# Kernel tuning notes

Measured on AMD Instinct MI355X. Metric: run time of the kernel, lower is better.

Reference implementation:

```python
import jax, jax.numpy as jnp
import numpy as np

NUM_HEADS = 8
EPS = 1e-3

N_TOKENS = 32768
DIM = 256
N_WIN = 128
WIN = N_TOKENS // N_WIN  # 256 tokens per window


def setup_inputs() -> dict:
    key = jax.random.key(0)
    ks = jax.random.split(key, 4)
    x = jax.random.normal(ks[0], (N_TOKENS, DIM), dtype=jnp.float32)
    # torch nn.Linear weights are [out_features, in_features]
    w_qkv = jax.random.normal(ks[1], (3 * DIM, DIM), dtype=jnp.float32) * (DIM ** -0.5)
    w_proj = jax.random.normal(ks[2], (DIM, DIM), dtype=jnp.float32) * (DIM ** -0.5)
    b_proj = jnp.zeros((DIM,), dtype=jnp.float32)
    batch_win_inds = (jnp.arange(N_TOKENS) // WIN).astype(jnp.int64)
    offsets = (jnp.arange(N_WIN) * WIN).astype(jnp.int64)
    counts = jnp.full((N_WIN,), WIN, dtype=jnp.int64)
    return {"x": x, "w_qkv": w_qkv, "w_proj": w_proj, "b_proj": b_proj,
            "offsets": offsets, "counts": counts, "batch_win_inds": batch_win_inds}


def reference(x, w_qkv, w_proj, b_proj, offsets, counts, batch_win_inds):
    N, C = x.shape
    H = NUM_HEADS
    hd = C // H
    W = counts.shape[0]  # number of windows (static)

    qkv = x @ w_qkv.T                      # [N, 3C]
    q, k, v = jnp.split(qkv, 3, axis=-1)   # each [N, C]
    q = jax.nn.relu(q.reshape(N, H, hd))   # [N, H, hd]
    k = jax.nn.relu(k.reshape(N, H, hd))
    v = v.reshape(N, H, hd)

    seg = batch_win_inds.astype(jnp.int32)
    # per-window KV state: kv[w] = sum_{i in w} k_i^T v_i   -> [W, H, hd, hd]
    kv = jax.ops.segment_sum(jnp.einsum('nhc,nhd->nhcd', k, v), seg, num_segments=W)
    # per-window key sum for normalizer                      -> [W, H, hd]
    s = jax.ops.segment_sum(k, seg, num_segments=W)

    y = jnp.einsum('nhc,nhcd->nhd', q, kv[seg])              # [N, H, hd]
    z = jnp.sum(s[seg] * q, axis=-1, keepdims=True)          # [N, H, 1]
    y = y / (z + EPS)

    y = y.reshape(N, C) @ w_proj.T + b_proj                  # [N, C]
    return y
```

## Files before the change

kernel.cpp:

```cpp
#include <hip/hip_runtime.h>

typedef __bf16 bf16_t;
typedef bf16_t bf16x8 __attribute__((ext_vector_type(8)));
typedef bf16_t bf16x4 __attribute__((ext_vector_type(4)));
typedef float f32x4 __attribute__((ext_vector_type(4)));

#define M_TOK 32768
#define NWIN 128
#define WIN  256

typedef __attribute__((address_space(3))) void* as3p;
typedef const __attribute__((address_space(1))) void* as1p;

__device__ __forceinline__ void gll16(const void* g, void* l) {
    __builtin_amdgcn_global_load_lds((as1p)g, (as3p)l, 16, 0, 0);
}

#define VMW_(n) asm volatile("s_waitcnt vmcnt(" #n ")" ::: "memory")
#define VMW(n) VMW_(n)

__global__ __launch_bounds__(256) void wconv(
    const float* __restrict__ wq, const float* __restrict__ wp,
    bf16_t* __restrict__ wqb, bf16_t* __restrict__ wpb)
{
    int i4 = (blockIdx.x * 256 + threadIdx.x) * 4;
    const float* s; bf16_t* dst; int idx;
    if (i4 < 196608) { s = wq; dst = wqb; idx = i4; }
    else             { s = wp; dst = wpb; idx = i4 - 196608; }
    f32x4 v = *(const f32x4*)(s + idx);
    bf16x4 o;
    o[0] = (bf16_t)v[0]; o[1] = (bf16_t)v[1]; o[2] = (bf16_t)v[2]; o[3] = (bf16_t)v[3];
    *(bf16x4*)(dst + idx) = o;
}

__global__ __launch_bounds__(512) void gemm1_qkv(
    const float* __restrict__ X,
    const bf16_t* __restrict__ Wb,
    bf16_t* __restrict__ QKV)
{
    __shared__ __align__(16) bf16_t Al[64][256];
    __shared__ __align__(16) bf16_t Bs[3][128][64];

    const int tid = threadIdx.x;
    const int lane = tid & 63;
    const int wv = tid >> 6;
    const int wm = wv >> 2, wn = wv & 3;
    const int m0 = blockIdx.x * 64;
    const int r = lane & 15, q = lane >> 4;
    const int rl = lane >> 3, gsl = lane & 7;

    f32x4 acc[2][2] = {};

    auto stageB = [&](int t) {
        const int nb = t >> 2, kc = (t & 3) * 64;
#pragma unroll
        for (int u = 0; u < 2; ++u)
            gll16(Wb + (size_t)(nb * 128 + wv * 16 + u * 8 + rl) * 256 + kc + (gsl ^ rl) * 8,
                  &Bs[t % 3][wv * 16 + u * 8][0]);
    };

    auto comp = [&](int t) {
        const int buf = t % 3;
#pragma unroll
        for (int s = 0; s < 2; ++s) {
            const int kk = (t & 3) * 2 + s;
            bf16x8 a[2], b[2];
#pragma unroll
            for (int i = 0; i < 2; ++i)
                a[i] = *(const bf16x8*)((const bf16_t*)Al +
                        (wm * 32 + i * 16 + r) * 256 + ((kk * 4 + q) ^ (r & 7)) * 8);
#pragma unroll
            for (int j = 0; j < 2; ++j)
                b[j] = *(const bf16x8*)&Bs[buf][wn * 32 + j * 16 + r][((s * 4 + q) ^ (r & 7)) * 8];
#pragma unroll
            for (int i = 0; i < 2; ++i)
#pragma unroll
                for (int j = 0; j < 2; ++j)
                    acc[i][j] = __builtin_amdgcn_mfma_f32_16x16x32_bf16(b[j], a[i], acc[i][j], 0, 0, 0);
        }
    };

    auto wout = [&](int nb) {
#pragma unroll
        for (int i = 0; i < 2; ++i) {
            const int rowg = m0 + wm * 32 + i * 16 + r;
#pragma unroll
            for (int j = 0; j < 2; ++j) {
                const int nbcol = nb * 128 + wn * 32 + j * 16 + q * 4;
                const int nblk = nbcol >> 5, d = nbcol & 31;
                bf16x4 o;
#pragma unroll
                for (int reg = 0; reg < 4; ++reg) {
                    float v = acc[i][j][reg];
                    if (nblk < 16) v = fmaxf(v, 0.0f);
                    o[reg] = (bf16_t)v;
                }
                *(bf16x4*)&QKV[((size_t)nblk * M_TOK + rowg) * 32 + d] = o;
                acc[i][j] = (f32x4){0.f, 0.f, 0.f, 0.f};
            }
        }
    };

    f32x4 av[8];
#pragma unroll
    for (int it = 0; it < 8; ++it) {
        const int L = it * 512 + tid;
        const int row = L >> 6, col4 = L & 63;
        av[it] = *(const f32x4*)(X + (size_t)(m0 + row) * 256 + col4 * 4);
    }
    __builtin_amdgcn_sched_barrier(0);
    stageB(0); stageB(1); stageB(2);
    __builtin_amdgcn_sched_barrier(0);
#pragma unroll
    for (int it = 0; it < 8; ++it) {
        const int L = it * 512 + tid;
        const int row = L >> 6, col4 = L & 63;
        bf16x4 o;
        o[0] = (bf16_t)av[it][0]; o[1] = (bf16_t)av[it][1];
        o[2] = (bf16_t)av[it][2]; o[3] = (bf16_t)av[it][3];
        const int gs = (col4 >> 1) ^ (row & 7);
        *(bf16x4*)((bf16_t*)Al + row * 256 + gs * 8 + (col4 & 1) * 4) = o;
    }
    asm volatile("s_waitcnt lgkmcnt(0)" ::: "memory");
    __builtin_amdgcn_s_barrier();

#define G1S(t, NW) do { \
        VMW(NW); \
        __builtin_amdgcn_s_barrier(); \
        __builtin_amdgcn_sched_barrier(0); \
        comp(t); \
        if (((t) & 3) == 3) wout((t) >> 2); \
        __builtin_amdgcn_sched_barrier(0); \
        __builtin_amdgcn_s_barrier(); \
        if ((t) + 3 < 24) stageB((t) + 3); \
    } while (0)

    G1S(0, 4);  G1S(1, 4);  G1S(2, 4);  G1S(3, 4);
    G1S(4, 4);  G1S(5, 4);  G1S(6, 4);  G1S(7, 4);
    G1S(8, 4);  G1S(9, 4);  G1S(10, 4); G1S(11, 4);
    G1S(12, 4); G1S(13, 4); G1S(14, 4); G1S(15, 4);
    G1S(16, 4); G1S(17, 4); G1S(18, 4); G1S(19, 4);
    G1S(20, 4); G1S(21, 4); G1S(22, 2); G1S(23, 0);
#undef G1S
}

__global__ __launch_bounds__(512) void gemm2_proj(
    const bf16_t* __restrict__ Y,
    const bf16_t* __restrict__ Wb,
    const float* __restrict__ bias,
    float* __restrict__ Out)
{
    __shared__ __align__(16) bf16_t Al[64][256];
    __shared__ __align__(16) bf16_t Bs[3][128][64];

    const int tid = threadIdx.x;
    const int lane = tid & 63;
    const int wv = tid >> 6;
    const int wm = wv >> 2, wn = wv & 3;
    const int m0 = blockIdx.x * 64;
    const int r = lane & 15, q = lane >> 4;
    const int rl = lane >> 3, gsl = lane & 7;

    f32x4 acc[2][2] = {};

    auto stageB = [&](int t) {
        const int nb = t >> 2, kc = (t & 3) * 64;
#pragma unroll
        for (int u = 0; u < 2; ++u)
            gll16(Wb + (size_t)(nb * 128 + wv * 16 + u * 8 + rl) * 256 + kc + (gsl ^ rl) * 8,
                  &Bs[t % 3][wv * 16 + u * 8][0]);
    };

    auto comp = [&](int t) {
        const int buf = t % 3;
#pragma unroll
        for (int s = 0; s < 2; ++s) {
            const int kk = (t & 3) * 2 + s;
            bf16x8 a[2], b[2];
#pragma unroll
            for (int i = 0; i < 2; ++i)
                a[i] = *(const bf16x8*)((const bf16_t*)Al +
                        (wm * 32 + i * 16 + r) * 256 + ((kk * 4 + q) ^ (r & 7)) * 8);
#pragma unroll
            for (int j = 0; j < 2; ++j)
                b[j] = *(const bf16x8*)&Bs[buf][wn * 32 + j * 16 + r][((s * 4 + q) ^ (r & 7)) * 8];
#pragma unroll
            for (int i = 0; i < 2; ++i)
#pragma unroll
                for (int j = 0; j < 2; ++j)
                    acc[i][j] = __builtin_amdgcn_mfma_f32_16x16x32_bf16(b[j], a[i], acc[i][j], 0, 0, 0);
        }
    };

    auto wout = [&](int nb) {
#pragma unroll
        for (int i = 0; i < 2; ++i) {
            const int rowg = m0 + wm * 32 + i * 16 + r;
#pragma unroll
            for (int j = 0; j < 2; ++j) {
                const int n = nb * 128 + wn * 32 + j * 16 + q * 4;
                f32x4 bi = *(const f32x4*)(bias + n);
                f32x4 o;
#pragma unroll
                for (int reg = 0; reg < 4; ++reg) o[reg] = acc[i][j][reg] + bi[reg];
                *(f32x4*)&Out[(size_t)rowg * 256 + n] = o;
                acc[i][j] = (f32x4){0.f, 0.f, 0.f, 0.f};
            }
        }
    };

#pragma unroll
    for (int u = 0; u < 4; ++u) {
        const int rowl = wv * 8 + u * 2 + (lane >> 5);
        const int gsrc = (lane & 31) ^ (rowl & 7);
        gll16(Y + (size_t)(m0 + rowl) * 256 + gsrc * 8, &Al[wv * 8 + u * 2][0]);
    }
    stageB(0); stageB(1); stageB(2);

#define G2S(t, NW) do { \
        VMW(NW); \
        __builtin_amdgcn_s_barrier(); \
        __builtin_amdgcn_sched_barrier(0); \
        comp(t); \
        if (((t) & 3) == 3) wout((t) >> 2); \
        __builtin_amdgcn_sched_barrier(0); \
        __builtin_amdgcn_s_barrier(); \
        if ((t) + 3 < 8) stageB((t) + 3); \
    } while (0)

    G2S(0, 4); G2S(1, 4); G2S(2, 4); G2S(3, 4);
    G2S(4, 4); G2S(5, 4); G2S(6, 2); G2S(7, 0);
#undef G2S
}

__global__ __launch_bounds__(256) void kvy_kernel(
    const bf16_t* __restrict__ QKV,
    const int* __restrict__ offsets,
    const int* __restrict__ counts,
    bf16_t* __restrict__ Y)
{
    const int w = blockIdx.x;
    const int h = blockIdx.y;
    const int is64 = (counts[1] == 0) ? 1 : 0;
    const int off = offsets[w << is64];
    const int tid = threadIdx.x;
    const int lane = tid & 63;
    const int wv = tid >> 6;

    __shared__ __align__(16) bf16_t KT[32 * 264];
    __shared__ __align__(16) bf16_t VT[32 * 264];
    __shared__ __align__(16) bf16_t KVT[32 * 40];
    __shared__ float sbuf[32];
    __shared__ float spart[32 * 8];
    __shared__ float zinv[WIN];

    {
        const int t = tid;
        const bf16_t* kp = QKV + ((size_t)(8 + h) * M_TOK + off + t) * 32;
        const bf16_t* vp = QKV + ((size_t)(16 + h) * M_TOK + off + t) * 32;
        bf16_t ka[32], va[32];
#pragma unroll
        for (int u = 0; u < 4; ++u) {
            bf16x8 kk = *(const bf16x8*)(kp + u * 8);
            bf16x8 vvv = *(const bf16x8*)(vp + u * 8);
#pragma unroll
            for (int j = 0; j < 8; ++j) { ka[u * 8 + j] = kk[j]; va[u * 8 + j] = vvv[j]; }
        }
#pragma unroll
        for (int c = 0; c < 32; ++c) {
            KT[c * 264 + t] = ka[c];
            VT[c * 264 + t] = va[c];
        }
    }
    __syncthreads();

    {
        const int c = tid >> 3;
        const int tc = (tid & 7) * 32;
        float ps = 0.f;
#pragma unroll
        for (int u = 0; u < 4; ++u) {
            bf16x8 kk = *(const bf16x8*)(&KT[c * 264 + tc + u * 8]);
#pragma unroll
            for (int j = 0; j < 8; ++j) ps += (float)kk[j];
        }
        spart[c * 8 + (tid & 7)] = ps;
    }
    {
        const int i = wv >> 1, j = wv & 1;
        const int r = lane & 15, q = lane >> 4;
        f32x4 acc = {};
#pragma unroll
        for (int ch = 0; ch < 8; ++ch) {
            bf16x8 af = *(const bf16x8*)(&KT[(i * 16 + r) * 264 + ch * 32 + q * 8]);
            bf16x8 bf_ = *(const bf16x8*)(&VT[(j * 16 + r) * 264 + ch * 32 + q * 8]);
            acc = __builtin_amdgcn_mfma_f32_16x16x32_bf16(af, bf_, acc, 0, 0, 0);
        }
        bf16x4 kv4;
#pragma unroll
        for (int reg = 0; reg < 4; ++reg) kv4[reg] = (bf16_t)acc[reg];
        *(bf16x4*)(&KVT[(j * 16 + r) * 40 + i * 16 + q * 4]) = kv4;
    }
    __syncthreads();
    if (tid < 32) {
        float s = 0.f;
#pragma unroll
        for (int u = 0; u < 8; ++u) s += spart[tid * 8 + u];
        sbuf[tid] = s;
    }
    __syncthreads();

    {
        const int t = tid;
        const bf16_t* qp = QKV + ((size_t)h * M_TOK + off + t) * 32;
        float z = 0.f;
#pragma unroll
        for (int u = 0; u < 4; ++u) {
            bf16x8 qq = *(const bf16x8*)(qp + u * 8);
#pragma unroll
            for (int j = 0; j < 8; ++j) z += (float)qq[j] * sbuf[u * 8 + j];
        }
        zinv[t] = 1.0f / (z + 1e-3f);
    }
    __syncthreads();

    {
        const int r = lane & 15, q = lane >> 4;
        bf16x8 b0 = *(const bf16x8*)(&KVT[(r) * 40 + q * 8]);
        bf16x8 b1 = *(const bf16x8*)(&KVT[(16 + r) * 40 + q * 8]);
#pragma unroll
        for (int u = 0; u < 4; ++u) {
            const int mi = wv * 4 + u;
            const bf16_t* ap = QKV + ((size_t)h * M_TOK + off + mi * 16 + r) * 32 + q * 8;
            bf16x8 af = *(const bf16x8*)ap;
            f32x4 acc0 = {}, acc1 = {};
            acc0 = __builtin_amdgcn_mfma_f32_16x16x32_bf16(b0, af, acc0, 0, 0, 0);
            acc1 = __builtin_amdgcn_mfma_f32_16x16x32_bf16(b1, af, acc1, 0, 0, 0);
            const int tkn = mi * 16 + r;
            const float zi = zinv[tkn];
            bf16_t* yp = Y + (size_t)(off + tkn) * 256 + h * 32;
            bf16x4 o0, o1;
#pragma unroll
            for (int reg = 0; reg < 4; ++reg) {
                o0[reg] = (bf16_t)(acc0[reg] * zi);
                o1[reg] = (bf16_t)(acc1[reg] * zi);
            }
            *(bf16x4*)(yp + q * 4) = o0;
            *(bf16x4*)(yp + 16 + q * 4) = o1;
        }
    }
}

extern "C" void kernel_launch(void* const* d_in, const int* in_sizes, int n_in,
                              void* d_out, int out_size, void* d_ws, size_t ws_size,
                              hipStream_t stream) {
    const float* x      = (const float*)d_in[0];
    const float* w_qkv  = (const float*)d_in[1];
    const float* w_proj = (const float*)d_in[2];
    const float* b_proj = (const float*)d_in[3];
    const int*   offs   = (const int*)d_in[4];
    const int*   cnts   = (const int*)d_in[5];

    char* ws = (char*)d_ws;
    bf16_t* QKV = (bf16_t*)ws;
    bf16_t* Y   = (bf16_t*)(ws + 50331648);
    bf16_t* Wqb = (bf16_t*)(ws + 67108864);
    bf16_t* Wpb = (bf16_t*)(ws + 67502080);
    float*  out = (float*)d_out;

    wconv<<<256, 256, 0, stream>>>(w_qkv, w_proj, Wqb, Wpb);

    gemm1_qkv<<<512, 512, 0, stream>>>(x, Wqb, QKV);

    kvy_kernel<<<dim3(NWIN, 8), 256, 0, stream>>>(QKV, offs, cnts, Y);

    gemm2_proj<<<512, 512, 0, stream>>>(Y, Wpb, b_proj, out);
}
```

Baseline: 138.1 us.

## Fuse QKV projection with per-window linear attention in one kernel

Replaces the QKV GEMM kernel and the per-window KV/Y kernel with a single fused kernel. Each block loads one 256-token window of X into LDS as bf16 and loops over four heads. Per head it computes Q, K and V with MFMA, builds the KV state and key sum in LDS, and writes Y directly. This removes the global round trip of the large bf16 QKV intermediate and one kernel launch. In exchange, X is loaded twice (once per half of the heads), the kernel uses about 160KB of LDS so only one block fits per CU, and the phases are serialized by many barriers.

```diff
diff --git a/kernel.cpp b/kernel.cpp
--- a/kernel.cpp
+++ b/kernel.cpp
@@ -18,6 +18,8 @@
 
 #define VMW_(n) asm volatile("s_waitcnt vmcnt(" #n ")" ::: "memory")
 #define VMW(n) VMW_(n)
+
+#define MFMA16(b, a, c) __builtin_amdgcn_mfma_f32_16x16x32_bf16((b), (a), (c), 0, 0, 0)
 
 __global__ __launch_bounds__(256) void wconv(
     const float* __restrict__ wq, const float* __restrict__ wp,
@@ -33,115 +35,183 @@
     *(bf16x4*)(dst + idx) = o;
 }
 
-__global__ __launch_bounds__(512) void gemm1_qkv(
+__global__ __launch_bounds__(512) void fused_attn(
     const float* __restrict__ X,
-    const bf16_t* __restrict__ Wb,
-    bf16_t* __restrict__ QKV)
+    const bf16_t* __restrict__ Wq,
+    const int* __restrict__ offsets,
+    const int* __restrict__ counts,
+    bf16_t* __restrict__ Y)
 {
-    __shared__ __align__(16) bf16_t Al[64][256];
-    __shared__ __align__(16) bf16_t Bs[3][128][64];
-
+    __shared__ __align__(16) bf16_t Xb[65536];
+    __shared__ __align__(16) bf16_t SCR[16384];
+
+    const int bid = blockIdx.x;
+    const int w  = (bid & 7) * 16 + (bid >> 4);
+    const int hh = (bid >> 3) & 1;
+    const int is64 = (counts[1] == 0) ? 1 : 0;
+    const int off = offsets[w << is64];
     const int tid = threadIdx.x;
     const int lane = tid & 63;
     const int wv = tid >> 6;
-    const int wm = wv >> 2, wn = wv & 3;
-    const int m0 = blockIdx.x * 64;
     const int r = lane & 15, q = lane >> 4;
-    const int rl = lane >> 3, gsl = lane & 7;
-
-    f32x4 acc[2][2] = {};
-
-    auto stageB = [&](int t) {
-        const int nb = t >> 2, kc = (t & 3) * 64;
-#pragma unroll
-        for (int u = 0; u < 2; ++u)
-            gll16(Wb + (size_t)(nb * 128 + wv * 16 + u * 8 + rl) * 256 + kc + (gsl ^ rl) * 8,
-                  &Bs[t % 3][wv * 16 + u * 8][0]);
-    };
-
-    auto comp = [&](int t) {
-        const int buf = t % 3;
-#pragma unroll
-        for (int s = 0; s < 2; ++s) {
-            const int kk = (t & 3) * 2 + s;
-            bf16x8 a[2], b[2];
-#pragma unroll
-            for (int i = 0; i < 2; ++i)
-                a[i] = *(const bf16x8*)((const bf16_t*)Al +
-                        (wm * 32 + i * 16 + r) * 256 + ((kk * 4 + q) ^ (r & 7)) * 8);
-#pragma unroll
-            for (int j = 0; j < 2; ++j)
-                b[j] = *(const bf16x8*)&Bs[buf][wn * 32 + j * 16 + r][((s * 4 + q) ^ (r & 7)) * 8];
-#pragma unroll
-            for (int i = 0; i < 2; ++i)
-#pragma unroll
-                for (int j = 0; j < 2; ++j)
-                    acc[i][j] = __builtin_amdgcn_mfma_f32_16x16x32_bf16(b[j], a[i], acc[i][j], 0, 0, 0);
-        }
-    };
-
-    auto wout = [&](int nb) {
-#pragma unroll
-        for (int i = 0; i < 2; ++i) {
-            const int rowg = m0 + wm * 32 + i * 16 + r;
-#pragma unroll
-            for (int j = 0; j < 2; ++j) {
-                const int nbcol = nb * 128 + wn * 32 + j * 16 + q * 4;
-                const int nblk = nbcol >> 5, d = nbcol & 31;
-                bf16x4 o;
-#pragma unroll
-                for (int reg = 0; reg < 4; ++reg) {
-                    float v = acc[i][j][reg];
-                    if (nblk < 16) v = fmaxf(v, 0.0f);
-                    o[reg] = (bf16_t)v;
-                }
-                *(bf16x4*)&QKV[((size_t)nblk * M_TOK + rowg) * 32 + d] = o;
-                acc[i][j] = (f32x4){0.f, 0.f, 0.f, 0.f};
-            }
-        }
-    };
-
-    f32x4 av[8];
-#pragma unroll
-    for (int it = 0; it < 8; ++it) {
+
+    bf16_t* Wl  = SCR;
+    bf16_t* KT  = SCR;
+    bf16_t* VT  = SCR + 8192;
+    bf16_t* Ql  = SCR;
+    bf16_t* kvb = SCR + 10240;
+    float*  sfp = (float*)(SCR + 11264);
+    float*  zin = (float*)(SCR + 11328);
+
+#pragma unroll 8
+    for (int it = 0; it < 32; ++it) {
         const int L = it * 512 + tid;
         const int row = L >> 6, col4 = L & 63;
-        av[it] = *(const f32x4*)(X + (size_t)(m0 + row) * 256 + col4 * 4);
+        f32x4 v = *(const f32x4*)(X + (size_t)(off + row) * 256 + col4 * 4);
+        bf16x4 o;
+        o[0] = (bf16_t)v[0]; o[1] = (bf16_t)v[1]; o[2] = (bf16_t)v[2]; o[3] = (bf16_t)v[3];
+        const int gs = (col4 >> 1) ^ (row & 7);
+        *(bf16x4*)(Xb + row * 256 + gs * 8 + (col4 & 1) * 4) = o;
     }
-    __builtin_amdgcn_sched_barrier(0);
-    stageB(0); stageB(1); stageB(2);
-    __builtin_amdgcn_sched_barrier(0);
-#pragma unroll
-    for (int it = 0; it < 8; ++it) {
-        const int L = it * 512 + tid;
-        const int row = L >> 6, col4 = L & 63;
-        bf16x4 o;
-        o[0] = (bf16_t)av[it][0]; o[1] = (bf16_t)av[it][1];
-        o[2] = (bf16_t)av[it][2]; o[3] = (bf16_t)av[it][3];
-        const int gs = (col4 >> 1) ^ (row & 7);
-        *(bf16x4*)((bf16_t*)Al + row * 256 + gs * 8 + (col4 & 1) * 4) = o;
+    __syncthreads();
+
+    for (int h4 = 0; h4 < 4; ++h4) {
+        const int h = hh * 4 + h4;
+
+#pragma unroll
+        for (int u = 0; u < 4; ++u) {
+            const int rowl = wv * 8 + u * 2 + (lane >> 5);
+            const size_t grow = (size_t)((wv < 4 ? 256 : 480) + h * 32 + rowl);
+            gll16(Wq + grow * 256 + ((lane & 31) ^ (rowl & 7)) * 8,
+                  Wl + (wv * 8 + u * 2) * 256);
+        }
+        __syncthreads();
+
+        f32x4 aQ[2][2] = {}, aK[2][2] = {}, aV[2][2] = {};
+#pragma unroll
+        for (int kch = 0; kch < 8; ++kch) {
+            const int slot8 = (((kch * 4 + q) ^ (r & 7)) * 8);
+            bf16x8 xa[2];
+#pragma unroll
+            for (int i2 = 0; i2 < 2; ++i2)
+                xa[i2] = *(const bf16x8*)(Xb + (wv * 32 + i2 * 16 + r) * 256 + slot8);
+#pragma unroll
+            for (int ct = 0; ct < 2; ++ct) {
+                bf16x8 bq = *(const bf16x8*)(Wq + (size_t)(h * 32 + ct * 16 + r) * 256
+                                              + kch * 32 + q * 8);
+                bf16x8 bk = *(const bf16x8*)(Wl + (ct * 16 + r) * 256 + slot8);
+                bf16x8 bv = *(const bf16x8*)(Wl + (32 + ct * 16 + r) * 256 + slot8);
+#pragma unroll
+                for (int i2 = 0; i2 < 2; ++i2) {
+                    aQ[i2][ct] = MFMA16(bq, xa[i2], aQ[i2][ct]);
+                    aK[i2][ct] = MFMA16(bk, xa[i2], aK[i2][ct]);
+                    aV[i2][ct] = MFMA16(bv, xa[i2], aV[i2][ct]);
+                }
+            }
+        }
+        __syncthreads();
+
+#pragma unroll
+        for (int i2 = 0; i2 < 2; ++i2) {
+            const int t = wv * 32 + i2 * 16 + r;
+            const int gt = t >> 3;
+#pragma unroll
+            for (int ct = 0; ct < 2; ++ct)
+#pragma unroll
+                for (int reg = 0; reg < 4; ++reg) {
+                    const int c = ct * 16 + q * 4 + reg;
+                    const int ei = c * 256 + (gt ^ (c & 7)) * 8 + (t & 7);
+                    KT[ei] = (bf16_t)fmaxf(aK[i2][ct][reg], 0.f);
+                    VT[ei] = (bf16_t)aV[i2][ct][reg];
+                }
+        }
+        __syncthreads();
+
+        f32x4 kva = {};
+        float sc = 0.f;
+        if (wv < 4) {
+            const int ct = wv >> 1, dt = wv & 1;
+#pragma unroll
+            for (int kch = 0; kch < 8; ++kch) {
+                const int slot8 = (((kch * 4 + q) ^ (r & 7)) * 8);
+                bf16x8 ak = *(const bf16x8*)(KT + (ct * 16 + r) * 256 + slot8);
+                bf16x8 bv = *(const bf16x8*)(VT + (dt * 16 + r) * 256 + slot8);
+                kva = MFMA16(bv, ak, kva);
+            }
+        } else {
+            const int tl = tid - 256;
+            const int c = tl >> 3, p = tl & 7;
+#pragma unroll
+            for (int g = 0; g < 4; ++g) {
+                bf16x8 kk = *(const bf16x8*)(KT + c * 256 + (p + g * 8) * 8);
+#pragma unroll
+                for (int j = 0; j < 8; ++j) sc += (float)kk[j];
+            }
+            sc += __shfl_xor(sc, 1);
+            sc += __shfl_xor(sc, 2);
+            sc += __shfl_xor(sc, 4);
+        }
+        __syncthreads();
+
+#pragma unroll
+        for (int i2 = 0; i2 < 2; ++i2) {
+            const int t = wv * 32 + i2 * 16 + r;
+#pragma unroll
+            for (int ct = 0; ct < 2; ++ct) {
+                bf16x4 o;
+#pragma unroll
+                for (int reg = 0; reg < 4; ++reg)
+                    o[reg] = (bf16_t)fmaxf(aQ[i2][ct][reg], 0.f);
+                *(bf16x4*)(Ql + t * 40 + ct * 16 + q * 4) = o;
+            }
+        }
+        if (wv < 4) {
+            const int ct = wv >> 1, dt = wv & 1;
+#pragma unroll
+            for (int reg = 0; reg < 4; ++reg)
+                kvb[(dt * 16 + q * 4 + reg) * 32 + ct * 16 + r] = (bf16_t)kva[reg];
+        } else {
+            const int tl = tid - 256;
+            if ((tl & 7) == 0) sfp[tl >> 3] = sc;
+        }
+        __syncthreads();
+
+        if (tid < 256) {
+            float z = 0.f;
+#pragma unroll
+            for (int g = 0; g < 4; ++g) {
+                bf16x8 qq = *(const bf16x8*)(Ql + tid * 40 + g * 8);
+#pragma unroll
+                for (int j = 0; j < 8; ++j) z += (float)qq[j] * sfp[g * 8 + j];
+            }
+            zin[tid] = 1.f / (z + 1e-3f);
+        }
+        __syncthreads();
+
+        {
+            bf16x8 bk0 = *(const bf16x8*)(kvb + r * 32 + q * 8);
+            bf16x8 bk1 = *(const bf16x8*)(kvb + (16 + r) * 32 + q * 8);
+#pragma unroll
+            for (int i2 = 0; i2 < 2; ++i2) {
+                const int t = wv * 32 + i2 * 16 + r;
+                bf16x8 aq = *(const bf16x8*)(Ql + t * 40 + q * 8);
+                f32x4 y0 = {}, y1 = {};
+                y0 = MFMA16(bk0, aq, y0);
+                y1 = MFMA16(bk1, aq, y1);
+                const float zi = zin[t];
+                bf16x4 o0, o1;
+#pragma unroll
+                for (int reg = 0; reg < 4; ++reg) {
+                    o0[reg] = (bf16_t)(y0[reg] * zi);
+                    o1[reg] = (bf16_t)(y1[reg] * zi);
+                }
+                bf16_t* yp = Y + (size_t)(off + t) * 256 + h * 32;
+                *(bf16x4*)(yp + q * 4) = o0;
+                *(bf16x4*)(yp + 16 + q * 4) = o1;
+            }
+        }
+        __syncthreads();
     }
-    asm volatile("s_waitcnt lgkmcnt(0)" ::: "memory");
-    __builtin_amdgcn_s_barrier();
-
-#define G1S(t, NW) do { \
-        VMW(NW); \
-        __builtin_amdgcn_s_barrier(); \
-        __builtin_amdgcn_sched_barrier(0); \
-        comp(t); \
-        if (((t) & 3) == 3) wout((t) >> 2); \
-        __builtin_amdgcn_sched_barrier(0); \
-        __builtin_amdgcn_s_barrier(); \
-        if ((t) + 3 < 24) stageB((t) + 3); \
-    } while (0)
-
-    G1S(0, 4);  G1S(1, 4);  G1S(2, 4);  G1S(3, 4);
-    G1S(4, 4);  G1S(5, 4);  G1S(6, 4);  G1S(7, 4);
-    G1S(8, 4);  G1S(9, 4);  G1S(10, 4); G1S(11, 4);
-    G1S(12, 4); G1S(13, 4); G1S(14, 4); G1S(15, 4);
-    G1S(16, 4); G1S(17, 4); G1S(18, 4); G1S(19, 4);
-    G1S(20, 4); G1S(21, 4); G1S(22, 2); G1S(23, 0);
-#undef G1S
 }
 
 __global__ __launch_bounds__(512) void gemm2_proj(
@@ -188,7 +258,7 @@
             for (int i = 0; i < 2; ++i)
 #pragma unroll
                 for (int j = 0; j < 2; ++j)
-                    acc[i][j] = __builtin_amdgcn_mfma_f32_16x16x32_bf16(b[j], a[i], acc[i][j], 0, 0, 0);
+                    acc[i][j] = MFMA16(b[j], a[i], acc[i][j]);
         }
     };
 
@@ -233,124 +303,6 @@
 #undef G2S
 }
 
-__global__ __launch_bounds__(256) void kvy_kernel(
-    const bf16_t* __restrict__ QKV,
-    const int* __restrict__ offsets,
-    const int* __restrict__ counts,
-    bf16_t* __restrict__ Y)
-{
-    const int w = blockIdx.x;
-    const int h = blockIdx.y;
-    const int is64 = (counts[1] == 0) ? 1 : 0;
-    const int off = offsets[w << is64];
-    const int tid = threadIdx.x;
-    const int lane = tid & 63;
-    const int wv = tid >> 6;
-
-    __shared__ __align__(16) bf16_t KT[32 * 264];
-    __shared__ __align__(16) bf16_t VT[32 * 264];
-    __shared__ __align__(16) bf16_t KVT[32 * 40];
-    __shared__ float sbuf[32];
-    __shared__ float spart[32 * 8];
-    __shared__ float zinv[WIN];
-
-    {
-        const int t = tid;
-        const bf16_t* kp = QKV + ((size_t)(8 + h) * M_TOK + off + t) * 32;
-        const bf16_t* vp = QKV + ((size_t)(16 + h) * M_TOK + off + t) * 32;
-        bf16_t ka[32], va[32];
-#pragma unroll
-        for (int u = 0; u < 4; ++u) {
-            bf16x8 kk = *(const bf16x8*)(kp + u * 8);
-            bf16x8 vvv = *(const bf16x8*)(vp + u * 8);
-#pragma unroll
-            for (int j = 0; j < 8; ++j) { ka[u * 8 + j] = kk[j]; va[u * 8 + j] = vvv[j]; }
-        }
-#pragma unroll
-        for (int c = 0; c < 32; ++c) {
-            KT[c * 264 + t] = ka[c];
-            VT[c * 264 + t] = va[c];
-        }
-    }
-    __syncthreads();
-
-    {
-        const int c = tid >> 3;
-        const int tc = (tid & 7) * 32;
-        float ps = 0.f;
-#pragma unroll
-        for (int u = 0; u < 4; ++u) {
-            bf16x8 kk = *(const bf16x8*)(&KT[c * 264 + tc + u * 8]);
-#pragma unroll
-            for (int j = 0; j < 8; ++j) ps += (float)kk[j];
-        }
-        spart[c * 8 + (tid & 7)] = ps;
-    }
-    {
-        const int i = wv >> 1, j = wv & 1;
-        const int r = lane & 15, q = lane >> 4;
-        f32x4 acc = {};
-#pragma unroll
-        for (int ch = 0; ch < 8; ++ch) {
-            bf16x8 af = *(const bf16x8*)(&KT[(i * 16 + r) * 264 + ch * 32 + q * 8]);
-            bf16x8 bf_ = *(const bf16x8*)(&VT[(j * 16 + r) * 264 + ch * 32 + q * 8]);
-            acc = __builtin_amdgcn_mfma_f32_16x16x32_bf16(af, bf_, acc, 0, 0, 0);
-        }
-        bf16x4 kv4;
-#pragma unroll
-        for (int reg = 0; reg < 4; ++reg) kv4[reg] = (bf16_t)acc[reg];
-        *(bf16x4*)(&KVT[(j * 16 + r) * 40 + i * 16 + q * 4]) = kv4;
-    }
-    __syncthreads();
-    if (tid < 32) {
-        float s = 0.f;
-#pragma unroll
-        for (int u = 0; u < 8; ++u) s += spart[tid * 8 + u];
-        sbuf[tid] = s;
-    }
-    __syncthreads();
-
-    {
-        const int t = tid;
-        const bf16_t* qp = QKV + ((size_t)h * M_TOK + off + t) * 32;
-        float z = 0.f;
-#pragma unroll
-        for (int u = 0; u < 4; ++u) {
-            bf16x8 qq = *(const bf16x8*)(qp + u * 8);
-#pragma unroll
-            for (int j = 0; j < 8; ++j) z += (float)qq[j] * sbuf[u * 8 + j];
-        }
-        zinv[t] = 1.0f / (z + 1e-3f);
-    }
-    __syncthreads();
-
-    {
-        const int r = lane & 15, q = lane >> 4;
-        bf16x8 b0 = *(const bf16x8*)(&KVT[(r) * 40 + q * 8]);
-        bf16x8 b1 = *(const bf16x8*)(&KVT[(16 + r) * 40 + q * 8]);
-#pragma unroll
-        for (int u = 0; u < 4; ++u) {
-            const int mi = wv * 4 + u;
-            const bf16_t* ap = QKV + ((size_t)h * M_TOK + off + mi * 16 + r) * 32 + q * 8;
-            bf16x8 af = *(const bf16x8*)ap;
-            f32x4 acc0 = {}, acc1 = {};
-            acc0 = __builtin_amdgcn_mfma_f32_16x16x32_bf16(b0, af, acc0, 0, 0, 0);
-            acc1 = __builtin_amdgcn_mfma_f32_16x16x32_bf16(b1, af, acc1, 0, 0, 0);
-            const int tkn = mi * 16 + r;
-            const float zi = zinv[tkn];
-            bf16_t* yp = Y + (size_t)(off + tkn) * 256 + h * 32;
-            bf16x4 o0, o1;
-#pragma unroll
-            for (int reg = 0; reg < 4; ++reg) {
-                o0[reg] = (bf16_t)(acc0[reg] * zi);
-                o1[reg] = (bf16_t)(acc1[reg] * zi);
-            }
-            *(bf16x4*)(yp + q * 4) = o0;
-            *(bf16x4*)(yp + 16 + q * 4) = o1;
-        }
-    }
-}
-
 extern "C" void kernel_launch(void* const* d_in, const int* in_sizes, int n_in,
                               void* d_out, int out_size, void* d_ws, size_t ws_size,
                               hipStream_t stream) {
@@ -362,7 +314,6 @@
     const int*   cnts   = (const int*)d_in[5];
 
     char* ws = (char*)d_ws;
-    bf16_t* QKV = (bf16_t*)ws;
     bf16_t* Y   = (bf16_t*)(ws + 50331648);
     bf16_t* Wqb = (bf16_t*)(ws + 67108864);
     bf16_t* Wpb = (bf16_t*)(ws + 67502080);
@@ -370,9 +321,7 @@
 
     wconv<<<256, 256, 0, stream>>>(w_qkv, w_proj, Wqb, Wpb);
 
-    gemm1_qkv<<<512, 512, 0, stream>>>(x, Wqb, QKV);
-
-    kvy_kernel<<<dim3(NWIN, 8), 256, 0, stream>>>(QKV, offs, cnts, Y);
+    fused_attn<<<256, 512, 0, stream>>>(x, Wqb, offs, cnts, Y);
 
     gemm2_proj<<<512, 512, 0, stream>>>(Y, Wpb, b_proj, out);
 }
```

Result: faster. 133.2 us (-3.6%).
